# Optimization experiments

Hardware: AMD Instinct MI355X
Metric: run time of the kernel (lower is better)

## Reference

```python
import jax, jax.numpy as jnp
import numpy as np

EPS = 1e-8
C_RGLRU = 8.0  # Griffin constant

def rmsnorm(x, w):
    rms = jnp.sqrt(jnp.mean(x * x, axis=-1, keepdims=True) + EPS)
    return w * (x / rms)

def causal_depthwise_conv(x, conv_w, conv_b):
    # x: [B,S,H], conv_w: [K,H] depthwise causal conv, left-padded
    K = conv_w.shape[0]
    S = x.shape[1]
    xp = jnp.pad(x, ((0, 0), (K - 1, 0), (0, 0)))
    y = sum(conv_w[k] * xp[:, k:k + S, :] for k in range(K))
    return y + conv_b

def rg_lru(x, ga_W, ga_b, gx_W, gx_b, a_param):
    # x: [B,S,H]. Griffin RG-LRU: h_t = a_t h_{t-1} + sqrt(1-a_t^2) (i_t * x_t)
    r = jax.nn.sigmoid(x @ ga_W + ga_b)          # recurrence gate
    i = jax.nn.sigmoid(x @ gx_W + gx_b)          # input gate
    log_a = -C_RGLRU * jax.nn.softplus(a_param) * r
    a = jnp.exp(log_a)
    mult = jnp.sqrt(-jnp.expm1(2.0 * log_a))     # sqrt(1 - a^2), stable
    b = mult * (i * x)
    def combine(c1, c2):
        a1, b1 = c1
        a2, b2 = c2
        return a1 * a2, a2 * b1 + b2
    _, h = jax.lax.associative_scan(combine, (a, b), axis=1)
    return h

def setup_inputs() -> dict:
    D, H, F, K, B, S = 2048, 2048, 6144, 4, 2, 2048
    key = jax.random.key(0)
    ks = jax.random.split(key, 16)
    def lin(k, fan_in, shape):
        return jax.random.normal(k, shape, jnp.float32) * (fan_in ** -0.5)
    return {
        "x": jax.random.normal(ks[0], (B, S, D), jnp.float32),
        "norm1_w": jnp.ones((D,), jnp.float32),
        "left_W": lin(ks[1], D, (D, H)), "left_b": jnp.zeros((H,), jnp.float32),
        "right_W": lin(ks[2], D, (D, H)), "right_b": jnp.zeros((H,), jnp.float32),
        "conv_w": lin(ks[3], K, (K, H)), "conv_b": jnp.zeros((H,), jnp.float32),
        "ga_W": lin(ks[4], H, (H, H)), "ga_b": jnp.zeros((H,), jnp.float32),
        "gx_W": lin(ks[5], H, (H, H)), "gx_b": jnp.zeros((H,), jnp.float32),
        "a_param": jax.random.uniform(ks[6], (H,), jnp.float32, 0.5, 3.0),
        "out_W": lin(ks[7], H, (H, D)), "out_b": jnp.zeros((D,), jnp.float32),
        "norm2_w": jnp.ones((D,), jnp.float32),
        "up1_W": lin(ks[8], D, (D, F)), "up1_b": jnp.zeros((F,), jnp.float32),
        "up2_W": lin(ks[9], D, (D, F)), "up2_b": jnp.zeros((F,), jnp.float32),
        "down_W": lin(ks[10], F, (F, D)), "down_b": jnp.zeros((D,), jnp.float32),
    }

def reference(x, norm1_w, left_W, left_b, right_W, right_b, conv_w, conv_b,
              ga_W, ga_b, gx_W, gx_b, a_param, out_W, out_b,
              norm2_w, up1_W, up1_b, up2_W, up2_b, down_W, down_b):
    gelu = lambda t: jax.nn.gelu(t, approximate=False)
    # recurrent sub-block (pre-norm residual)
    xn = rmsnorm(x, norm1_w)
    left = gelu(xn @ left_W + left_b)
    right = rg_lru(causal_depthwise_conv(xn @ right_W + right_b, conv_w, conv_b),
                   ga_W, ga_b, gx_W, gx_b, a_param)
    x1 = (left * right) @ out_W + out_b + x
    # gated MLP sub-block (pre-norm residual)
    x1n = rmsnorm(x1, norm2_w)
    mlp = (gelu(x1n @ up1_W + up1_b) * (x1n @ up2_W + up2_b)) @ down_W + down_b
    return mlp + x1
```

## Files before the change

kernel.cpp:

```cpp
#include <hip/hip_runtime.h>
#include <cstdint>
#include <cstdio>

typedef __bf16 bf16x8 __attribute__((ext_vector_type(8)));
typedef float  f32x4  __attribute__((ext_vector_type(4)));
typedef const __attribute__((address_space(1))) void* gas_ptr;
typedef __attribute__((address_space(3))) void* las_ptr;

__device__ __forceinline__ uint16_t f32_to_bf16_rne(float f){
  uint32_t u = __builtin_bit_cast(uint32_t, f);
  u += 0x7FFFu + ((u >> 16) & 1u);
  return (uint16_t)(u >> 16);
}
__device__ __forceinline__ float bf16_to_f32(uint16_t h){
  uint32_t u = (uint32_t)h << 16;
  return __builtin_bit_cast(float, u);
}
__device__ __forceinline__ float gelu_exact(float x){
  return 0.5f * x * (1.f + erff(x * 0.7071067811865475f));
}

template<int EPI, int BM>
__global__ __launch_bounds__(512, 2)
void gemm8(const uint16_t* __restrict__ A, const uint16_t* __restrict__ Bt,
           const float* __restrict__ bias0, const float* __restrict__ bias1,
           const float* __restrict__ auxF, const uint16_t* __restrict__ auxB,
           float* __restrict__ Cf, uint16_t* __restrict__ Cb0, uint16_t* __restrict__ Cb1,
           int M, int N, int K, int SPLIT)
{
  constexpr int BN = 256;
  constexpr int M_REP = BM / 32;
  constexpr int MH    = M_REP / 2;
  constexpr int LOADS_A = BM / 64;
  constexpr int LOADS_B = BN / 64;
  constexpr int LTOT  = LOADS_A + LOADS_B;
  constexpr int ABYTES = 2 * BM * 128;
  __shared__ alignas(16) char smem[(2 * (BM + BN)) * 128];

  const int tid  = threadIdx.x;
  const int wid  = tid >> 6;
  const int lane = tid & 63;
  const int wm = wid >> 2, wn = wid & 3;
  const int la = lane & 15, lq = lane >> 4;
  const int n0 = blockIdx.x * BN;
  const int m0 = blockIdx.y * BM;

  const int rt = tid >> 3, ct = tid & 7;
  const int gs = ct ^ (rt & 7);
  const uint16_t* srcA = A  + (size_t)(m0 + rt) * K + gs * 8;
  const uint16_t* srcB = Bt + (size_t)(n0 + rt) * K + gs * 8;

  const int rowAb = (wm * (BM / 2) + la) * 128;
  const int rowBb = (wn * 64 + la) * 128;
  const int ck0 = ((lq)     ^ (la & 7)) * 16;
  const int ck1 = ((4 + lq) ^ (la & 7)) * 16;

  f32x4 acc[M_REP][4];
  const f32x4 fz = {0.f, 0.f, 0.f, 0.f};
#pragma unroll
  for (int m = 0; m < M_REP; ++m)
#pragma unroll
    for (int n = 0; n < 4; ++n) acc[m][n] = fz;

  bf16x8 aF[MH][2];
  bf16x8 bF[2][2][2];

  const int NT = K >> 6;

#define STAGE(KT, CUR) do {                                                   \
    const uint16_t* sa_ = srcA + (size_t)(KT) * 64;                           \
    const uint16_t* sb_ = srcB + (size_t)(KT) * 64;                           \
    _Pragma("unroll")                                                         \
    for (int l = 0; l < LOADS_A; ++l)                                         \
      __builtin_amdgcn_global_load_lds((gas_ptr)(sa_ + (size_t)l * 64 * K),   \
          (las_ptr)(smem + (CUR) * BM * 128 + (l * 512 + tid) * 16), 16, 0, 0);\
    _Pragma("unroll")                                                         \
    for (int l = 0; l < LOADS_B; ++l)                                         \
      __builtin_amdgcn_global_load_lds((gas_ptr)(sb_ + (size_t)l * 64 * K),   \
          (las_ptr)(smem + ABYTES + (CUR) * BN * 128 + (l * 512 + tid) * 16), \
          16, 0, 0);                                                          \
  } while (0)

#define LDA(MHS, CUR) do {                                                    \
    _Pragma("unroll")                                                         \
    for (int mq = 0; mq < MH; ++mq) {                                         \
      int ro_ = (CUR) * BM * 128 + rowAb + ((MHS) * MH + mq) * 2048;          \
      aF[mq][0] = *(const bf16x8*)(smem + ro_ + ck0);                         \
      aF[mq][1] = *(const bf16x8*)(smem + ro_ + ck1);                         \
    }                                                                         \
  } while (0)

#define LDB(NH, CUR) do {                                                     \
    _Pragma("unroll")                                                         \
    for (int nq = 0; nq < 2; ++nq) {                                          \
      int ro_ = ABYTES + (CUR) * BN * 128 + rowBb + ((NH) * 2 + nq) * 2048;   \
      bF[NH][nq][0] = *(const bf16x8*)(smem + ro_ + ck0);                     \
      bF[NH][nq][1] = *(const bf16x8*)(smem + ro_ + ck1);                     \
    }                                                                         \
  } while (0)

#define MM(MHS, NH) do {                                                      \
    _Pragma("unroll")                                                         \
    for (int mq = 0; mq < MH; ++mq)                                           \
      _Pragma("unroll")                                                       \
      for (int nq = 0; nq < 2; ++nq) {                                        \
        acc[(MHS)*MH+mq][(NH)*2+nq] = __builtin_amdgcn_mfma_f32_16x16x32_bf16(\
            aF[mq][0], bF[NH][nq][0], acc[(MHS)*MH+mq][(NH)*2+nq], 0, 0, 0);  \
        acc[(MHS)*MH+mq][(NH)*2+nq] = __builtin_amdgcn_mfma_f32_16x16x32_bf16(\
            aF[mq][1], bF[NH][nq][1], acc[(MHS)*MH+mq][(NH)*2+nq], 0, 0, 0);  \
      }                                                                       \
  } while (0)

#define BARR()  __builtin_amdgcn_s_barrier()
#define SCH()   __builtin_amdgcn_sched_barrier(0)
#define LGKM0() asm volatile("s_waitcnt lgkmcnt(0)" ::: "memory")

  STAGE(0, 0);
  STAGE(1, 1);
  asm volatile("s_waitcnt vmcnt(%0)" :: "i"(LTOT) : "memory");
  BARR(); SCH();

  for (int kt = 0; kt < NT; ++kt) {
    const int cur = kt & 1;
    LDB(0, cur); LDA(0, cur);
    SCH(); BARR(); LGKM0(); SCH();
    __builtin_amdgcn_s_setprio(1); MM(0, 0); __builtin_amdgcn_s_setprio(0);
    SCH(); BARR(); SCH();
    LDB(1, cur);
    SCH(); BARR(); LGKM0(); SCH();
    __builtin_amdgcn_s_setprio(1); MM(0, 1); __builtin_amdgcn_s_setprio(0);
    SCH(); BARR(); SCH();
    LDA(1, cur);
    SCH(); BARR(); LGKM0(); SCH();
    __builtin_amdgcn_s_setprio(1); MM(1, 0); __builtin_amdgcn_s_setprio(0);
    SCH(); BARR(); SCH();
    if (kt + 2 < NT) STAGE(kt + 2, cur);
    SCH(); BARR(); LGKM0(); SCH();
    __builtin_amdgcn_s_setprio(1); MM(1, 1); __builtin_amdgcn_s_setprio(0);
    SCH();
    if (kt + 2 < NT) asm volatile("s_waitcnt vmcnt(%0)" :: "i"(LTOT) : "memory");
    else             asm volatile("s_waitcnt vmcnt(0)" ::: "memory");
    BARR(); SCH();
  }

#undef STAGE
#undef LDA
#undef LDB
#undef MM
#undef BARR
#undef SCH
#undef LGKM0

#pragma unroll
  for (int n = 0; n < 4; ++n) {
    int col = n0 + wn * 64 + n * 16 + la;
    const bool second = (col >= SPLIT);
    float bv = second ? bias1[col - SPLIT] : bias0[col];
#pragma unroll
    for (int m = 0; m < M_REP; ++m) {
      int rbase = m0 + wm * (BM / 2) + m * 16 + lq * 4;
#pragma unroll
      for (int r = 0; r < 4; ++r) {
        int row = rbase + r;
        size_t idx = (size_t)row * N + col;
        float v = acc[m][n][r] + bv;
        if constexpr (EPI == 0) Cf[idx] = v + auxF[idx];
        if constexpr (EPI == 1) {
          if (!second) Cb0[(size_t)row * SPLIT + col] = f32_to_bf16_rne(gelu_exact(v));
          else         Cb1[(size_t)row * (N - SPLIT) + (col - SPLIT)] = f32_to_bf16_rne(v);
        }
        if constexpr (EPI == 2) Cb0[idx] = f32_to_bf16_rne(v);
        if constexpr (EPI == 3) Cb0[idx] = f32_to_bf16_rne(v * bf16_to_f32(auxB[idx]));
      }
    }
  }
}

__global__ __launch_bounds__(256)
void cvt_transpose(const float* __restrict__ in, uint16_t* __restrict__ out, int R, int C)
{
  __shared__ float tile[64][65];
  const int r0 = blockIdx.y * 64, c0 = blockIdx.x * 64;
  const int t = threadIdx.x;
  const int lc = (t & 15) * 4;
  const int lr0 = t >> 4;
#pragma unroll
  for (int j = 0; j < 4; j++){
    int lr = lr0 + j*16;
    float4 v = *(const float4*)(in + (size_t)(r0 + lr) * C + c0 + lc);
    tile[lr][lc+0] = v.x; tile[lr][lc+1] = v.y; tile[lr][lc+2] = v.z; tile[lr][lc+3] = v.w;
  }
  __syncthreads();
  const int oc = t >> 2;
  const int rseg = (t & 3) * 16;
  alignas(16) uint16_t tmp[16];
#pragma unroll
  for (int j = 0; j < 16; j++) tmp[j] = f32_to_bf16_rne(tile[rseg + j][oc]);
  uint4* dst = (uint4*)(out + (size_t)(c0 + oc) * R + r0 + rseg);
  dst[0] = *(const uint4*)(&tmp[0]);
  dst[1] = *(const uint4*)(&tmp[8]);
}

__global__ __launch_bounds__(256)
void rmsnorm_kernel(const float* __restrict__ x, const float* __restrict__ w,
                    uint16_t* __restrict__ out, int D)
{
  const int row = blockIdx.x;
  const float* xr = x + (size_t)row * D;
  const int base = threadIdx.x * 8;
  float4 va = *(const float4*)(xr + base);
  float4 vb = *(const float4*)(xr + base + 4);
  float ss = va.x*va.x + va.y*va.y + va.z*va.z + va.w*va.w
           + vb.x*vb.x + vb.y*vb.y + vb.z*vb.z + vb.w*vb.w;
#pragma unroll
  for (int o = 32; o > 0; o >>= 1) ss += __shfl_xor(ss, o);
  __shared__ float red[4];
  if ((threadIdx.x & 63) == 0) red[threadIdx.x >> 6] = ss;
  __syncthreads();
  float tot = red[0] + red[1] + red[2] + red[3];
  float inv = rsqrtf(tot / (float)D + 1e-8f);
  float4 wa = *(const float4*)(w + base);
  float4 wb = *(const float4*)(w + base + 4);
  alignas(16) uint16_t tmp[8];
  tmp[0] = f32_to_bf16_rne(va.x * wa.x * inv);
  tmp[1] = f32_to_bf16_rne(va.y * wa.y * inv);
  tmp[2] = f32_to_bf16_rne(va.z * wa.z * inv);
  tmp[3] = f32_to_bf16_rne(va.w * wa.w * inv);
  tmp[4] = f32_to_bf16_rne(vb.x * wb.x * inv);
  tmp[5] = f32_to_bf16_rne(vb.y * wb.y * inv);
  tmp[6] = f32_to_bf16_rne(vb.z * wb.z * inv);
  tmp[7] = f32_to_bf16_rne(vb.w * wb.w * inv);
  *(uint4*)(out + (size_t)row * D + base) = *(const uint4*)tmp;
}

__global__ __launch_bounds__(256)
void conv_kernel(const uint16_t* __restrict__ xin, const float* __restrict__ cw,
                 const float* __restrict__ cb, uint16_t* __restrict__ yout,
                 int S, int H)
{
  const int h = blockIdx.x * 256 + threadIdx.x;
  const int b = blockIdx.z;
  const int t0 = blockIdx.y * 128;
  const float w0 = cw[h], w1 = cw[H + h], w2 = cw[2*H + h], w3 = cw[3*H + h];
  const float bias = cb[h];
  const size_t colbase = (size_t)b * S * H + h;
  float xm3 = (t0 >= 3) ? bf16_to_f32(xin[colbase + (size_t)(t0-3)*H]) : 0.f;
  float xm2 = (t0 >= 2) ? bf16_to_f32(xin[colbase + (size_t)(t0-2)*H]) : 0.f;
  float xm1 = (t0 >= 1) ? bf16_to_f32(xin[colbase + (size_t)(t0-1)*H]) : 0.f;
  for (int t = t0; t < t0 + 128; ++t){
    size_t idx = colbase + (size_t)t * H;
    float xt = bf16_to_f32(xin[idx]);
    float y = w0*xm3 + w1*xm2 + w2*xm1 + w3*xt + bias;
    yout[idx] = f32_to_bf16_rne(y);
    xm3 = xm2; xm2 = xm1; xm1 = xt;
  }
}

__device__ __forceinline__ void rglru_ab(float rp, float ip, float xc, float coef,
                                         float& a, float& bb)
{
  float r  = 1.f / (1.f + expf(-rp));
  float la = coef * r;
  a = expf(la);
  float mult = sqrtf(-expm1f(2.f * la));
  float ig = 1.f / (1.f + expf(-ip));
  bb = mult * ig * xc;
}

__global__ __launch_bounds__(256)
void scan_phase1(const uint16_t* __restrict__ gpre, const uint16_t* __restrict__ convb,
                 const float* __restrict__ ap,
                 float* __restrict__ SA, float* __restrict__ SB,
                 int S, int H, int T0, int NC)
{
  const int h = blockIdx.x * 256 + threadIdx.x;
  const int j = blockIdx.y, b = blockIdx.z;
  const float coef = -8.f * log1pf(expf(ap[h]));
  size_t rowb = (size_t)b * S + (size_t)j * T0;
  float A = 1.f, Bc = 0.f;
  for (int t = 0; t < T0; ++t){
    size_t row = rowb + t;
    float rp = bf16_to_f32(gpre[row * 2 * H + h]);
    float ip = bf16_to_f32(gpre[row * 2 * H + H + h]);
    float xc = bf16_to_f32(convb[row * H + h]);
    float a, bb; rglru_ab(rp, ip, xc, coef, a, bb);
    A *= a; Bc = a * Bc + bb;
  }
  size_t o = ((size_t)b * NC + j) * H + h;
  SA[o] = A; SB[o] = Bc;
}

__global__ __launch_bounds__(256)
void scan_phase2(const float* __restrict__ SA, const float* __restrict__ SB,
                 float* __restrict__ SH, int H, int NC)
{
  const int h = blockIdx.x * 256 + threadIdx.x;
  const int b = blockIdx.y;
  float hh = 0.f;
  for (int j = 0; j < NC; ++j){
    size_t o = ((size_t)b * NC + j) * H + h;
    SH[o] = hh;
    hh = SA[o] * hh + SB[o];
  }
}

__global__ __launch_bounds__(256)
void scan_phase3(const uint16_t* __restrict__ gpre, const uint16_t* __restrict__ convb,
                 const float* __restrict__ ap, const float* __restrict__ SH,
                 const uint16_t* __restrict__ left, uint16_t* __restrict__ lr,
                 int S, int H, int T0, int NC)
{
  const int h = blockIdx.x * 256 + threadIdx.x;
  const int j = blockIdx.y, b = blockIdx.z;
  const float coef = -8.f * log1pf(expf(ap[h]));
  float hh = SH[((size_t)b * NC + j) * H + h];
  size_t rowb = (size_t)b * S + (size_t)j * T0;
  for (int t = 0; t < T0; ++t){
    size_t row = rowb + t;
    float rp = bf16_to_f32(gpre[row * 2 * H + h]);
    float ip = bf16_to_f32(gpre[row * 2 * H + H + h]);
    float xc = bf16_to_f32(convb[row * H + h]);
    float a, bb; rglru_ab(rp, ip, xc, coef, a, bb);
    hh = a * hh + bb;
    lr[row * H + h] = f32_to_bf16_rne(bf16_to_f32(left[row * H + h]) * hh);
  }
}

extern "C" void kernel_launch(void* const* d_in, const int* in_sizes, int n_in,
                              void* d_out, int out_size, void* d_ws, size_t ws_size,
                              hipStream_t stream)
{
  const int B = 2, S = 2048, D = 2048, H = 2048, F = 6144;
  const int M = B * S;
  const int NC = 32, T0 = S / NC;

  const float* x       = (const float*)d_in[0];
  const float* norm1_w = (const float*)d_in[1];
  const float* left_W  = (const float*)d_in[2];
  const float* left_b  = (const float*)d_in[3];
  const float* right_W = (const float*)d_in[4];
  const float* right_b = (const float*)d_in[5];
  const float* conv_w  = (const float*)d_in[6];
  const float* conv_b  = (const float*)d_in[7];
  const float* ga_W    = (const float*)d_in[8];
  const float* ga_b    = (const float*)d_in[9];
  const float* gx_W    = (const float*)d_in[10];
  const float* gx_b    = (const float*)d_in[11];
  const float* a_param = (const float*)d_in[12];
  const float* out_W   = (const float*)d_in[13];
  const float* out_b   = (const float*)d_in[14];
  const float* norm2_w = (const float*)d_in[15];
  const float* up1_W   = (const float*)d_in[16];
  const float* up1_b   = (const float*)d_in[17];
  const float* up2_W   = (const float*)d_in[18];
  const float* up2_b   = (const float*)d_in[19];
  const float* down_W  = (const float*)d_in[20];
  const float* down_b  = (const float*)d_in[21];

  char* ws = (char*)d_ws;
  size_t off = 0;
  auto alloc = [&](size_t bytes) -> char* {
    char* p = ws + off; off += (bytes + 255) & ~(size_t)255; return p;
  };
  uint16_t* WT    = (uint16_t*)alloc((size_t)F * D * 2);
  uint16_t* XN    = (uint16_t*)alloc((size_t)M * D * 2);
  uint16_t* LEFT  = (uint16_t*)alloc((size_t)M * H * 2);
  uint16_t* RPRE  = (uint16_t*)alloc((size_t)M * H * 2);
  uint16_t* CONVB = (uint16_t*)alloc((size_t)M * H * 2);
  uint16_t* GPRE  = (uint16_t*)alloc((size_t)M * 2 * H * 2);
  uint16_t* LR    = (uint16_t*)alloc((size_t)M * H * 2);
  float*    X1    = (float*)   alloc((size_t)M * D * 4);
  uint16_t* X1N   = (uint16_t*)alloc((size_t)M * D * 2);
  float*    SA    = (float*)   alloc((size_t)B * NC * H * 4);
  float*    SB    = (float*)   alloc((size_t)B * NC * H * 4);
  float*    SHB   = (float*)   alloc((size_t)B * NC * H * 4);
  uint16_t* T1    = XN;
  uint16_t* G     = CONVB;

  if (off > ws_size) {
    fprintf(stderr, "kernel_launch: ws too small, need %zu have %zu\n", off, ws_size);
    return;
  }

  float* OUT = (float*)d_out;
  dim3 blk(256);
  dim3 gblk(512);

  rmsnorm_kernel<<<M, blk, 0, stream>>>(x, norm1_w, XN, D);

  cvt_transpose<<<dim3(H/64, D/64), blk, 0, stream>>>(left_W, WT, D, H);
  cvt_transpose<<<dim3(H/64, D/64), blk, 0, stream>>>(right_W, WT + (size_t)H * D, D, H);
  gemm8<1, 256><<<dim3((2*H)/256, M/256), gblk, 0, stream>>>(
      XN, WT, left_b, right_b, nullptr, nullptr, nullptr, LEFT, RPRE, M, 2*H, D, H);

  conv_kernel<<<dim3(H/256, S/128, B), blk, 0, stream>>>(RPRE, conv_w, conv_b, CONVB, S, H);

  cvt_transpose<<<dim3(H/64, H/64), blk, 0, stream>>>(ga_W, WT, H, H);
  cvt_transpose<<<dim3(H/64, H/64), blk, 0, stream>>>(gx_W, WT + (size_t)H * H, H, H);
  gemm8<2, 256><<<dim3((2*H)/256, M/256), gblk, 0, stream>>>(
      CONVB, WT, ga_b, gx_b, nullptr, nullptr, nullptr, GPRE, nullptr, M, 2*H, H, H);

  scan_phase1<<<dim3(H/256, NC, B), blk, 0, stream>>>(GPRE, CONVB, a_param, SA, SB, S, H, T0, NC);
  scan_phase2<<<dim3(H/256, B), blk, 0, stream>>>(SA, SB, SHB, H, NC);
  scan_phase3<<<dim3(H/256, NC, B), blk, 0, stream>>>(GPRE, CONVB, a_param, SHB, LEFT, LR, S, H, T0, NC);

  cvt_transpose<<<dim3(D/64, H/64), blk, 0, stream>>>(out_W, WT, H, D);
  gemm8<0, 128><<<dim3(D/256, M/128), gblk, 0, stream>>>(
      LR, WT, out_b, out_b, x, nullptr, X1, nullptr, nullptr, M, D, H, D);

  rmsnorm_kernel<<<M, blk, 0, stream>>>(X1, norm2_w, X1N, D);

  cvt_transpose<<<dim3(F/64, D/64), blk, 0, stream>>>(up1_W, WT, D, F);
  gemm8<1, 256><<<dim3(F/256, M/256), gblk, 0, stream>>>(
      X1N, WT, up1_b, up1_b, nullptr, nullptr, nullptr, T1, nullptr, M, F, D, F);

  cvt_transpose<<<dim3(F/64, D/64), blk, 0, stream>>>(up2_W, WT, D, F);
  gemm8<3, 256><<<dim3(F/256, M/256), gblk, 0, stream>>>(
      X1N, WT, up2_b, up2_b, nullptr, T1, nullptr, G, nullptr, M, F, D, F);

  cvt_transpose<<<dim3(D/64, F/64), blk, 0, stream>>>(down_W, WT, F, D);
  gemm8<0, 128><<<dim3(D/256, M/128), gblk, 0, stream>>>(
      G, WT, down_b, down_b, X1, nullptr, OUT, nullptr, nullptr, M, D, F, D);
}
```

Before: 902.6 us.

## Remap GEMM workgroups across XCDs and split A/B prefetch across sub-steps

Workgroup IDs are remapped so that consecutive tiles land on the same XCD when the grid size is a multiple of 8, aiming for better L2 reuse of shared A/B panels. The global-to-LDS prefetch is split into separate A and B stages. The B stage is now issued one MFMA sub-step earlier, once B's current buffer has been fully read, which spreads memory traffic across the loop. The explicit sched_barrier fences are removed, giving the compiler more freedom to interleave instructions, at the risk of less predictable scheduling around the LDS reads.

Result: faster. 864.2 us (-4.3%).

```diff
diff --git a/kernel.cpp b/kernel.cpp
--- a/kernel.cpp
+++ b/kernel.cpp
@@ -38,15 +38,20 @@
   __shared__ alignas(16) char smem[(2 * (BM + BN)) * 128];
 
   const int tid  = threadIdx.x;
+  const int lane = tid & 63;
   const int wid  = tid >> 6;
-  const int lane = tid & 63;
   const int wm = wid >> 2, wn = wid & 3;
   const int la = lane & 15, lq = lane >> 4;
-  const int n0 = blockIdx.x * BN;
-  const int m0 = blockIdx.y * BM;
-
-  const int rt = tid >> 3, ct = tid & 7;
-  const int gs = ct ^ (rt & 7);
+
+  const int gx = gridDim.x;
+  int bid = blockIdx.y * gx + blockIdx.x;
+  const int nwg = gx * gridDim.y;
+  if ((nwg & 7) == 0) bid = (bid & 7) * (nwg >> 3) + (bid >> 3);
+  const int n0 = (bid % gx) * BN;
+  const int m0 = (bid / gx) * BM;
+
+  const int rt = tid >> 3;
+  const int gs = (tid & 7) ^ (rt & 7);
   const uint16_t* srcA = A  + (size_t)(m0 + rt) * K + gs * 8;
   const uint16_t* srcB = Bt + (size_t)(n0 + rt) * K + gs * 8;
 
@@ -67,13 +72,16 @@
 
   const int NT = K >> 6;
 
-#define STAGE(KT, CUR) do {                                                   \
+#define STAGE_A(KT, CUR) do {                                                 \
     const uint16_t* sa_ = srcA + (size_t)(KT) * 64;                           \
-    const uint16_t* sb_ = srcB + (size_t)(KT) * 64;                           \
     _Pragma("unroll")                                                         \
     for (int l = 0; l < LOADS_A; ++l)                                         \
       __builtin_amdgcn_global_load_lds((gas_ptr)(sa_ + (size_t)l * 64 * K),   \
           (las_ptr)(smem + (CUR) * BM * 128 + (l * 512 + tid) * 16), 16, 0, 0);\
+  } while (0)
+
+#define STAGE_B(KT, CUR) do {                                                 \
+    const uint16_t* sb_ = srcB + (size_t)(KT) * 64;                           \
     _Pragma("unroll")                                                         \
     for (int l = 0; l < LOADS_B; ++l)                                         \
       __builtin_amdgcn_global_load_lds((gas_ptr)(sb_ + (size_t)l * 64 * K),   \
@@ -112,43 +120,43 @@
   } while (0)
 
 #define BARR()  __builtin_amdgcn_s_barrier()
-#define SCH()   __builtin_amdgcn_sched_barrier(0)
 #define LGKM0() asm volatile("s_waitcnt lgkmcnt(0)" ::: "memory")
 
-  STAGE(0, 0);
-  STAGE(1, 1);
+  STAGE_A(0, 0); STAGE_B(0, 0);
+  STAGE_A(1, 1); STAGE_B(1, 1);
   asm volatile("s_waitcnt vmcnt(%0)" :: "i"(LTOT) : "memory");
-  BARR(); SCH();
+  BARR();
 
   for (int kt = 0; kt < NT; ++kt) {
     const int cur = kt & 1;
+    const bool pf = (kt + 2 < NT);
     LDB(0, cur); LDA(0, cur);
-    SCH(); BARR(); LGKM0(); SCH();
+    BARR(); LGKM0();
     __builtin_amdgcn_s_setprio(1); MM(0, 0); __builtin_amdgcn_s_setprio(0);
-    SCH(); BARR(); SCH();
+    BARR();
     LDB(1, cur);
-    SCH(); BARR(); LGKM0(); SCH();
+    BARR(); LGKM0();
     __builtin_amdgcn_s_setprio(1); MM(0, 1); __builtin_amdgcn_s_setprio(0);
-    SCH(); BARR(); SCH();
+    BARR();
     LDA(1, cur);
-    SCH(); BARR(); LGKM0(); SCH();
+    if (pf) STAGE_B(kt + 2, cur);
+    BARR(); LGKM0();
     __builtin_amdgcn_s_setprio(1); MM(1, 0); __builtin_amdgcn_s_setprio(0);
-    SCH(); BARR(); SCH();
-    if (kt + 2 < NT) STAGE(kt + 2, cur);
-    SCH(); BARR(); LGKM0(); SCH();
+    BARR();
+    if (pf) STAGE_A(kt + 2, cur);
+    BARR(); LGKM0();
     __builtin_amdgcn_s_setprio(1); MM(1, 1); __builtin_amdgcn_s_setprio(0);
-    SCH();
-    if (kt + 2 < NT) asm volatile("s_waitcnt vmcnt(%0)" :: "i"(LTOT) : "memory");
-    else             asm volatile("s_waitcnt vmcnt(0)" ::: "memory");
-    BARR(); SCH();
-  }
-
-#undef STAGE
+    if (pf) asm volatile("s_waitcnt vmcnt(%0)" :: "i"(LTOT) : "memory");
+    else    asm volatile("s_waitcnt vmcnt(0)" ::: "memory");
+    BARR();
+  }
+
+#undef STAGE_A
+#undef STAGE_B
 #undef LDA
 #undef LDB
 #undef MM
 #undef BARR
-#undef SCH
 #undef LGKM0
 
 #pragma unroll
```

## Replace 8-wave ping-pong GEMM schedule with simple double-buffered prefetch loop

Applied to the files above, without the earlier changes.

Swaps the GEMM main loop's hand-interleaved schedule for a plain double-buffered loop. The old loop kept two tiles in flight, split the work into four LDS-load/MFMA phases separated by barriers and sched_barriers, and used occupancy hint 2. The new loop prefetches only the next tile, reads all fragments for a tile, runs the MFMAs, then waits on vmcnt(0) and one barrier. The aim is to cut barrier and scheduling overhead, but it gives up the deeper load/compute overlap and the occupancy hint, which can expose global load latency.

New measurement: 819.3 us. 1.1x faster.

```diff
diff --git a/kernel.cpp b/kernel.cpp
--- a/kernel.cpp
+++ b/kernel.cpp
@@ -21,32 +21,30 @@
 }
 
 template<int EPI, int BM>
-__global__ __launch_bounds__(512, 2)
-void gemm8(const uint16_t* __restrict__ A, const uint16_t* __restrict__ Bt,
-           const float* __restrict__ bias0, const float* __restrict__ bias1,
-           const float* __restrict__ auxF, const uint16_t* __restrict__ auxB,
-           float* __restrict__ Cf, uint16_t* __restrict__ Cb0, uint16_t* __restrict__ Cb1,
-           int M, int N, int K, int SPLIT)
+__global__ __launch_bounds__(512)
+void gemm2p(const uint16_t* __restrict__ A, const uint16_t* __restrict__ Bt,
+            const float* __restrict__ bias0, const float* __restrict__ bias1,
+            const float* __restrict__ auxF, const uint16_t* __restrict__ auxB,
+            float* __restrict__ Cf, uint16_t* __restrict__ Cb0, uint16_t* __restrict__ Cb1,
+            int M, int N, int K, int SPLIT)
 {
   constexpr int BN = 256;
-  constexpr int M_REP = BM / 32;
-  constexpr int MH    = M_REP / 2;
+  constexpr int M_REP   = BM / 32;
   constexpr int LOADS_A = BM / 64;
   constexpr int LOADS_B = BN / 64;
-  constexpr int LTOT  = LOADS_A + LOADS_B;
-  constexpr int ABYTES = 2 * BM * 128;
-  __shared__ alignas(16) char smem[(2 * (BM + BN)) * 128];
+  constexpr int ABYTES  = 2 * BM * 128;
+  __shared__ alignas(16) char smem[2 * (BM + BN) * 128];
 
   const int tid  = threadIdx.x;
+  const int lane = tid & 63;
   const int wid  = tid >> 6;
-  const int lane = tid & 63;
   const int wm = wid >> 2, wn = wid & 3;
   const int la = lane & 15, lq = lane >> 4;
   const int n0 = blockIdx.x * BN;
   const int m0 = blockIdx.y * BM;
 
-  const int rt = tid >> 3, ct = tid & 7;
-  const int gs = ct ^ (rt & 7);
+  const int rt = tid >> 3;
+  const int gs = (tid & 7) ^ (rt & 7);
   const uint16_t* srcA = A  + (size_t)(m0 + rt) * K + gs * 8;
   const uint16_t* srcB = Bt + (size_t)(n0 + rt) * K + gs * 8;
 
@@ -62,94 +60,62 @@
 #pragma unroll
     for (int n = 0; n < 4; ++n) acc[m][n] = fz;
 
-  bf16x8 aF[MH][2];
-  bf16x8 bF[2][2][2];
-
   const int NT = K >> 6;
 
-#define STAGE(KT, CUR) do {                                                   \
+#define STAGE(KT, BUF) do {                                                   \
     const uint16_t* sa_ = srcA + (size_t)(KT) * 64;                           \
     const uint16_t* sb_ = srcB + (size_t)(KT) * 64;                           \
     _Pragma("unroll")                                                         \
     for (int l = 0; l < LOADS_A; ++l)                                         \
       __builtin_amdgcn_global_load_lds((gas_ptr)(sa_ + (size_t)l * 64 * K),   \
-          (las_ptr)(smem + (CUR) * BM * 128 + (l * 512 + tid) * 16), 16, 0, 0);\
+          (las_ptr)(smem + (BUF) * BM * 128 + (l * 512 + tid) * 16), 16, 0, 0);\
     _Pragma("unroll")                                                         \
     for (int l = 0; l < LOADS_B; ++l)                                         \
       __builtin_amdgcn_global_load_lds((gas_ptr)(sb_ + (size_t)l * 64 * K),   \
-          (las_ptr)(smem + ABYTES + (CUR) * BN * 128 + (l * 512 + tid) * 16), \
+          (las_ptr)(smem + ABYTES + (BUF) * BN * 128 + (l * 512 + tid) * 16), \
           16, 0, 0);                                                          \
   } while (0)
 
-#define LDA(MHS, CUR) do {                                                    \
-    _Pragma("unroll")                                                         \
-    for (int mq = 0; mq < MH; ++mq) {                                         \
-      int ro_ = (CUR) * BM * 128 + rowAb + ((MHS) * MH + mq) * 2048;          \
-      aF[mq][0] = *(const bf16x8*)(smem + ro_ + ck0);                         \
-      aF[mq][1] = *(const bf16x8*)(smem + ro_ + ck1);                         \
-    }                                                                         \
-  } while (0)
-
-#define LDB(NH, CUR) do {                                                     \
-    _Pragma("unroll")                                                         \
-    for (int nq = 0; nq < 2; ++nq) {                                          \
-      int ro_ = ABYTES + (CUR) * BN * 128 + rowBb + ((NH) * 2 + nq) * 2048;   \
-      bF[NH][nq][0] = *(const bf16x8*)(smem + ro_ + ck0);                     \
-      bF[NH][nq][1] = *(const bf16x8*)(smem + ro_ + ck1);                     \
-    }                                                                         \
-  } while (0)
-
-#define MM(MHS, NH) do {                                                      \
-    _Pragma("unroll")                                                         \
-    for (int mq = 0; mq < MH; ++mq)                                           \
-      _Pragma("unroll")                                                       \
-      for (int nq = 0; nq < 2; ++nq) {                                        \
-        acc[(MHS)*MH+mq][(NH)*2+nq] = __builtin_amdgcn_mfma_f32_16x16x32_bf16(\
-            aF[mq][0], bF[NH][nq][0], acc[(MHS)*MH+mq][(NH)*2+nq], 0, 0, 0);  \
-        acc[(MHS)*MH+mq][(NH)*2+nq] = __builtin_amdgcn_mfma_f32_16x16x32_bf16(\
-            aF[mq][1], bF[NH][nq][1], acc[(MHS)*MH+mq][(NH)*2+nq], 0, 0, 0);  \
-      }                                                                       \
-  } while (0)
-
-#define BARR()  __builtin_amdgcn_s_barrier()
-#define SCH()   __builtin_amdgcn_sched_barrier(0)
-#define LGKM0() asm volatile("s_waitcnt lgkmcnt(0)" ::: "memory")
-
   STAGE(0, 0);
-  STAGE(1, 1);
-  asm volatile("s_waitcnt vmcnt(%0)" :: "i"(LTOT) : "memory");
-  BARR(); SCH();
-
+  asm volatile("s_waitcnt vmcnt(0)" ::: "memory");
+  __builtin_amdgcn_s_barrier();
+
+  int cur = 0;
   for (int kt = 0; kt < NT; ++kt) {
-    const int cur = kt & 1;
-    LDB(0, cur); LDA(0, cur);
-    SCH(); BARR(); LGKM0(); SCH();
-    __builtin_amdgcn_s_setprio(1); MM(0, 0); __builtin_amdgcn_s_setprio(0);
-    SCH(); BARR(); SCH();
-    LDB(1, cur);
-    SCH(); BARR(); LGKM0(); SCH();
-    __builtin_amdgcn_s_setprio(1); MM(0, 1); __builtin_amdgcn_s_setprio(0);
-    SCH(); BARR(); SCH();
-    LDA(1, cur);
-    SCH(); BARR(); LGKM0(); SCH();
-    __builtin_amdgcn_s_setprio(1); MM(1, 0); __builtin_amdgcn_s_setprio(0);
-    SCH(); BARR(); SCH();
-    if (kt + 2 < NT) STAGE(kt + 2, cur);
-    SCH(); BARR(); LGKM0(); SCH();
-    __builtin_amdgcn_s_setprio(1); MM(1, 1); __builtin_amdgcn_s_setprio(0);
-    SCH();
-    if (kt + 2 < NT) asm volatile("s_waitcnt vmcnt(%0)" :: "i"(LTOT) : "memory");
-    else             asm volatile("s_waitcnt vmcnt(0)" ::: "memory");
-    BARR(); SCH();
-  }
-
+    const bool pf = (kt + 1 < NT);
+    if (pf) STAGE(kt + 1, cur ^ 1);
+
+    const char* bufA = smem + cur * BM * 128;
+    const char* bufB = smem + ABYTES + cur * BN * 128;
+
+    bf16x8 bF[4][2];
+#pragma unroll
+    for (int n = 0; n < 4; ++n) {
+      int ro = (int)(bufB - smem) + rowBb + n * 2048;
+      bF[n][0] = *(const bf16x8*)(smem + ro + ck0);
+      bF[n][1] = *(const bf16x8*)(smem + ro + ck1);
+    }
+    __builtin_amdgcn_s_setprio(1);
+#pragma unroll
+    for (int m = 0; m < M_REP; ++m) {
+      int ro = (int)(bufA - smem) + rowAb + m * 2048;
+      bf16x8 a0 = *(const bf16x8*)(smem + ro + ck0);
+      bf16x8 a1 = *(const bf16x8*)(smem + ro + ck1);
+#pragma unroll
+      for (int n = 0; n < 4; ++n) {
+        acc[m][n] = __builtin_amdgcn_mfma_f32_16x16x32_bf16(a0, bF[n][0], acc[m][n], 0, 0, 0);
+        acc[m][n] = __builtin_amdgcn_mfma_f32_16x16x32_bf16(a1, bF[n][1], acc[m][n], 0, 0, 0);
+      }
+    }
+    __builtin_amdgcn_s_setprio(0);
+
+    if (pf) {
+      asm volatile("s_waitcnt vmcnt(0)" ::: "memory");
+      __builtin_amdgcn_s_barrier();
+      cur ^= 1;
+    }
+  }
 #undef STAGE
-#undef LDA
-#undef LDB
-#undef MM
-#undef BARR
-#undef SCH
-#undef LGKM0
 
 #pragma unroll
   for (int n = 0; n < 4; ++n) {
@@ -390,14 +356,14 @@
 
   cvt_transpose<<<dim3(H/64, D/64), blk, 0, stream>>>(left_W, WT, D, H);
   cvt_transpose<<<dim3(H/64, D/64), blk, 0, stream>>>(right_W, WT + (size_t)H * D, D, H);
-  gemm8<1, 256><<<dim3((2*H)/256, M/256), gblk, 0, stream>>>(
+  gemm2p<1, 256><<<dim3((2*H)/256, M/256), gblk, 0, stream>>>(
       XN, WT, left_b, right_b, nullptr, nullptr, nullptr, LEFT, RPRE, M, 2*H, D, H);
 
   conv_kernel<<<dim3(H/256, S/128, B), blk, 0, stream>>>(RPRE, conv_w, conv_b, CONVB, S, H);
 
   cvt_transpose<<<dim3(H/64, H/64), blk, 0, stream>>>(ga_W, WT, H, H);
   cvt_transpose<<<dim3(H/64, H/64), blk, 0, stream>>>(gx_W, WT + (size_t)H * H, H, H);
-  gemm8<2, 256><<<dim3((2*H)/256, M/256), gblk, 0, stream>>>(
+  gemm2p<2, 256><<<dim3((2*H)/256, M/256), gblk, 0, stream>>>(
       CONVB, WT, ga_b, gx_b, nullptr, nullptr, nullptr, GPRE, nullptr, M, 2*H, H, H);
 
   scan_phase1<<<dim3(H/256, NC, B), blk, 0, stream>>>(GPRE, CONVB, a_param, SA, SB, S, H, T0, NC);
@@ -405,20 +371,20 @@
   scan_phase3<<<dim3(H/256, NC, B), blk, 0, stream>>>(GPRE, CONVB, a_param, SHB, LEFT, LR, S, H, T0, NC);
 
   cvt_transpose<<<dim3(D/64, H/64), blk, 0, stream>>>(out_W, WT, H, D);
-  gemm8<0, 128><<<dim3(D/256, M/128), gblk, 0, stream>>>(
+  gemm2p<0, 128><<<dim3(D/256, M/128), gblk, 0, stream>>>(
       LR, WT, out_b, out_b, x, nullptr, X1, nullptr, nullptr, M, D, H, D);
 
   rmsnorm_kernel<<<M, blk, 0, stream>>>(X1, norm2_w, X1N, D);
 
   cvt_transpose<<<dim3(F/64, D/64), blk, 0, stream>>>(up1_W, WT, D, F);
-  gemm8<1, 256><<<dim3(F/256, M/256), gblk, 0, stream>>>(
+  gemm2p<1, 256><<<dim3(F/256, M/256), gblk, 0, stream>>>(
       X1N, WT, up1_b, up1_b, nullptr, nullptr, nullptr, T1, nullptr, M, F, D, F);
 
   cvt_transpose<<<dim3(F/64, D/64), blk, 0, stream>>>(up2_W, WT, D, F);
-  gemm8<3, 256><<<dim3(F/256, M/256), gblk, 0, stream>>>(
+  gemm2p<3, 256><<<dim3(F/256, M/256), gblk, 0, stream>>>(
       X1N, WT, up2_b, up2_b, nullptr, T1, nullptr, G, nullptr, M, F, D, F);
 
   cvt_transpose<<<dim3(D/64, F/64), blk, 0, stream>>>(down_W, WT, F, D);
-  gemm8<0, 128><<<dim3(D/256, M/128), gblk, 0, stream>>>(
+  gemm2p<0, 128><<<dim3(D/256, M/128), gblk, 0, stream>>>(
       G, WT, down_b, down_b, X1, nullptr, OUT, nullptr, nullptr, M, D, F, D);
 }
```
